# Optimization experiments

Hardware: AMD Instinct MI355X
Metric: run time of the kernel (lower is better)

Reference implementation:

```python
import jax, jax.numpy as jnp
import numpy as np

B, S, R = 8192, 256, 8192  # gas cells, species, reactions


def setup_inputs() -> dict:
    key = jax.random.key(0)
    ks = jax.random.split(key, 10)
    abundances = jax.random.uniform(ks[0], (B, S), jnp.float32, 1e-12, 1.0)
    temperature = jax.random.uniform(ks[1], (B,), jnp.float32, 10.0, 300.0)
    cr_rate = jax.random.uniform(ks[2], (B,), jnp.float32, 0.1, 10.0)
    fuv_rate = jax.random.uniform(ks[3], (B,), jnp.float32, 0.1, 10.0)
    time = jnp.zeros((B,), jnp.float32)  # unused by the RHS, kept for signature parity
    incidence = jax.random.normal(ks[4], (S, R), jnp.float32)  # stoichiometry matrix
    alpha = jax.random.uniform(ks[5], (R,), jnp.float32, 1e-12, 1e-9)
    beta = jax.random.normal(ks[6], (R,), jnp.float32) * 0.5
    gamma = jax.random.uniform(ks[7], (R,), jnp.float32, 0.0, 100.0)
    # species index or S (== out-of-bounds sentinel -> fill_value 1.0, i.e. <2 reactants)
    reactant_multipliers = jax.random.randint(ks[8], (R, 2), 0, S + 1, jnp.int32)
    rtype = jax.random.randint(ks[9], (R,), 0, 3, jnp.int32)  # 0: Arrhenius, 1: CR, 2: FUV
    return {
        'time': time, 'abundances': abundances, 'temperature': temperature,
        'cr_rate': cr_rate, 'fuv_rate': fuv_rate, 'incidence': incidence,
        'alpha': alpha, 'beta': beta, 'gamma': gamma,
        'reactant_multipliers': reactant_multipliers, 'rtype': rtype,
    }


def _get_rates(temperature, cr_rate, fuv_rate, alpha, beta, gamma, rtype):
    # JNetwork.get_rates: hstack of per-reaction rate terms -> (B, R)
    T = temperature[:, None]                                      # (B, 1)
    k_arr = alpha * jnp.exp(beta * jnp.log(T / 300.0) - gamma / T)  # Arrhenius
    k_cr = alpha * cr_rate[:, None]                               # cosmic-ray driven
    k_fuv = alpha * jnp.exp(-gamma) * fuv_rate[:, None]           # FUV photorate
    return jnp.where(rtype == 0, k_arr, jnp.where(rtype == 1, k_cr, k_fuv))


def reference(time, abundances, temperature, cr_rate, fuv_rate,
              incidence, alpha, beta, gamma, reactant_multipliers, rtype):
    rates = _get_rates(temperature, cr_rate, fuv_rate, alpha, beta, gamma, rtype)
    # multiply_rates_by_abundance: gather reactant abundances (mode='drop',
    # fill_value=1.0) and reduce with a product over the 2 reactant slots.
    ones_col = jnp.ones((abundances.shape[0], 1), abundances.dtype)
    ab_pad = jnp.concatenate([abundances, ones_col], axis=1)      # (B, S+1), col S == 1.0
    prod = ab_pad[:, reactant_multipliers[:, 0]] * ab_pad[:, reactant_multipliers[:, 1]]  # (B, R)
    flux = rates * prod                                           # (B, R)
    # incidence @ rates, batched: (S, R) x (B, R) -> (B, S)
    return jnp.einsum('sr,br->bs', incidence, flux)
```

## Files before the change

kernel.cpp:

```cpp
#include <hip/hip_runtime.h>
#include <stdint.h>

typedef __bf16 bf16;
typedef __bf16 bf16x8 __attribute__((ext_vector_type(8)));
typedef float  f32x4  __attribute__((ext_vector_type(4)));

#if __has_builtin(__builtin_amdgcn_exp2f)
#define EXP2F(x) __builtin_amdgcn_exp2f(x)
#else
#define EXP2F(x) exp2f(x)
#endif

constexpr int Bn = 8192, Sn = 256, Rn = 8192;
constexpr int BM = 64, BK = 32, KP = 4;
constexpr int KLEN = Rn / KP;
constexpr int NC = KLEN / BK;

__global__ __launch_bounds__(256) void prep_all(
    const float* __restrict__ inc, bf16* __restrict__ incb,
    const float* __restrict__ alpha, const float* __restrict__ beta,
    const float* __restrict__ gam, const int* __restrict__ rm, const int* __restrict__ rtype,
    float4* __restrict__ params, const float* __restrict__ temp,
    const float* __restrict__ cr, const float* __restrict__ fuv, float4* __restrict__ perb) {
  __shared__ __align__(16) float row_lds[8192];
  __shared__ unsigned short perm_lds[8192];
  __shared__ int c0[256], c1[256], c2[256];
  const int g = blockIdx.x, t = threadIdx.x;

  int* rt = (int*)row_lds;
  {
    const int4* src = (const int4*)rtype;
    int4* dst = (int4*)rt;
#pragma unroll
    for (int i = 0; i < 8; ++i) dst[i * 256 + t] = src[i * 256 + t];
  }
  __syncthreads();

  int ty[32];
  int l0 = 0, l1 = 0, l2 = 0;
#pragma unroll
  for (int i = 0; i < 32; ++i) {
    int v = rt[i * 256 + t];
    ty[i] = v;
    l0 += (v == 0); l1 += (v == 1); l2 += (v == 2);
  }
  c0[t] = l0; c1[t] = l1; c2[t] = l2;
  __syncthreads();
  for (int off = 1; off < 256; off <<= 1) {
    int a = (t >= off) ? c0[t - off] : 0;
    int b = (t >= off) ? c1[t - off] : 0;
    int c = (t >= off) ? c2[t - off] : 0;
    __syncthreads();
    c0[t] += a; c1[t] += b; c2[t] += c;
    __syncthreads();
  }
  const int tot0 = c0[255], tot1 = c1[255];
  int o0 = c0[t] - l0;
  int o1 = tot0 + c1[t] - l1;
  int o2 = tot0 + tot1 + c2[t] - l2;
#pragma unroll
  for (int i = 0; i < 32; ++i) {
    int v = ty[i];
    int pos = (v == 0) ? o0++ : ((v == 1) ? o1++ : o2++);
    perm_lds[pos] = (unsigned short)(i * 256 + t);
  }
  __syncthreads();

  if (g < 32) {
    int p = g * 256 + t;
    int r = perm_lds[p];
    float a = alpha[r], be = beta[r], gm = gam[r];
    int tv = rt[r];
    int i0 = rm[2 * r], i1 = rm[2 * r + 1];
    float x, P = 0.0f, Q = 0.0f;
    if (tv == 0) { x = __log2f(a); P = be; Q = gm; }
    else if (tv == 1) { x = a; }
    else { x = a * expf(-gm); }
    uint32_t bits = (uint32_t)i0 | ((uint32_t)i1 << 10) | ((uint32_t)tv << 20);
    params[p] = make_float4(x, P, Q, __uint_as_float(bits));
  } else if (g < 64) {
    int b = (g - 32) * 256 + t;
    float T = temp[b];
    perb[b] = make_float4(__log2f(T * (1.0f / 300.0f)), 1.4426950408889634f / T,
                          cr[b], fuv[b]);
  }
  __syncthreads();

  {
    const float4* src = (const float4*)(inc + ((size_t)g << 13));
    float4* dst = (float4*)row_lds;
#pragma unroll
    for (int i = 0; i < 8; ++i) dst[i * 256 + t] = src[i * 256 + t];
  }
  __syncthreads();

  const unsigned short* pp = perm_lds + t * 32;
  bf16* outp = incb + ((size_t)t * 256 + g) * 32;
#pragma unroll
  for (int k8 = 0; k8 < 4; ++k8) {
    bf16x8 o;
#pragma unroll
    for (int i = 0; i < 8; ++i) o[i] = (bf16)row_lds[pp[k8 * 8 + i]];
    *(bf16x8*)(outp + k8 * 8) = o;
  }
}

__global__ __launch_bounds__(256, 2) void flux_gemm(
    const float* __restrict__ abund, const float4* __restrict__ perb,
    const float4* __restrict__ params, const bf16* __restrict__ incb,
    float* __restrict__ partial) {
  __shared__ bf16 ab_lds[257 * 64];
  __shared__ bf16 flux_lds[2][64 * BK];

  const int tid  = threadIdx.x;
  const int lane = tid & 63;
  const int w    = tid >> 6;
  const int ws   = __builtin_amdgcn_readfirstlane(w);
  const int x   = blockIdx.x & 7;
  const int jb  = blockIdx.x >> 3;
  const int kp  = x & 3;
  const int m0g = (jb * 2 + (x >> 2)) * BM;
  const int kstart = kp * KLEN;
  const int r16 = lane & 15, q = lane >> 4;
  const int sw16 = (r16 >> 1) & 3;
  const int fsw  = w ^ ((lane >> 1) & 3);

  float4 pr0[8];
  {
    const float4* pw = params + kstart + ws * 8;
#pragma unroll
    for (int j = 0; j < 8; ++j) pr0[j] = pw[j];
  }

  {
    int bsub = tid >> 2;
    int scol = (tid & 3) * 64;
    const float* rowp = abund + (size_t)(m0g + bsub) * Sn + scol;
#pragma unroll
    for (int j = 0; j < 16; ++j) {
      float4 v = *(const float4*)(rowp + j * 4);
      int s = scol + j * 4;
      ab_lds[(s + 0) * 64 + bsub] = (bf16)v.x;
      ab_lds[(s + 1) * 64 + bsub] = (bf16)v.y;
      ab_lds[(s + 2) * 64 + bsub] = (bf16)v.z;
      ab_lds[(s + 3) * 64 + bsub] = (bf16)v.w;
    }
    if (tid < 64) ab_lds[256 * 64 + tid] = (bf16)1.0f;
  }

  float4 pb = perb[m0g + lane];
  const float l2t = pb.x, nitv = -pb.y, crv = pb.z, fuvv = pb.w;

  auto flux_tile = [&](int buf, const float4* pr) {
    uint32_t b0 = __builtin_amdgcn_readfirstlane(__float_as_uint(pr[0].w));
    uint32_t b7 = __builtin_amdgcn_readfirstlane(__float_as_uint(pr[7].w));
    uint32_t t0 = b0 >> 20, t7 = b7 >> 20;
    bf16x8 fv;
    if (t0 == 0 && t7 == 0) {
#pragma unroll
      for (int j = 0; j < 8; ++j) {
        uint32_t bits = __builtin_amdgcn_readfirstlane(__float_as_uint(pr[j].w));
        int i0 = (int)(bits & 1023), i1 = (int)((bits >> 10) & 1023);
        float a0 = (float)ab_lds[i0 * 64 + lane];
        float a1 = (float)ab_lds[i1 * 64 + lane];
        float v = EXP2F(fmaf(pr[j].y, l2t, fmaf(pr[j].z, nitv, pr[j].x)));
        fv[j] = (bf16)(v * (a0 * a1));
      }
    } else if (t0 == t7) {
      float mv = (t0 == 1) ? crv : fuvv;
#pragma unroll
      for (int j = 0; j < 8; ++j) {
        uint32_t bits = __builtin_amdgcn_readfirstlane(__float_as_uint(pr[j].w));
        int i0 = (int)(bits & 1023), i1 = (int)((bits >> 10) & 1023);
        float a0 = (float)ab_lds[i0 * 64 + lane];
        float a1 = (float)ab_lds[i1 * 64 + lane];
        fv[j] = (bf16)((pr[j].x * mv) * (a0 * a1));
      }
    } else {
#pragma unroll
      for (int j = 0; j < 8; ++j) {
        uint32_t bits = __builtin_amdgcn_readfirstlane(__float_as_uint(pr[j].w));
        int i0 = (int)(bits & 1023), i1 = (int)((bits >> 10) & 1023), ms = (int)(bits >> 20);
        float a0 = (float)ab_lds[i0 * 64 + lane];
        float a1 = (float)ab_lds[i1 * 64 + lane];
        float ve = EXP2F(fmaf(pr[j].y, l2t, fmaf(pr[j].z, nitv, pr[j].x)));
        float vm = pr[j].x * ((ms == 1) ? crv : fuvv);
        float v = (ms == 0) ? ve : vm;
        fv[j] = (bf16)(v * (a0 * a1));
      }
    }
    *(bf16x8*)(flux_lds[buf] + lane * BK + fsw * 8) = fv;
  };

  auto load_params = [&](int chunk, float4* pr) {
    const float4* pw = params + kstart + chunk * BK + ws * 8;
#pragma unroll
    for (int j = 0; j < 8; ++j) pr[j] = pw[j];
  };

  const bf16* bbase = incb + (size_t)(kstart / BK) * 8192 + (w * 64 + r16) * BK + q * 8;
  auto load_bfr = [&](int chunk, bf16x8* bfr) {
    const bf16* bp = bbase + (size_t)chunk * 8192;
#pragma unroll
    for (int nt = 0; nt < 4; ++nt)
      bfr[nt] = *(const bf16x8*)(bp + nt * (16 * BK));
  };

  auto do_mfma = [&](f32x4 (*acc)[4], const bf16x8* af, const bf16x8* bfr) {
    __builtin_amdgcn_s_setprio(1);
#pragma unroll
    for (int mt = 0; mt < 4; ++mt)
#pragma unroll
      for (int nt = 0; nt < 4; ++nt)
        acc[mt][nt] = __builtin_amdgcn_mfma_f32_16x16x32_bf16(af[mt], bfr[nt], acc[mt][nt], 0, 0, 0);
    __builtin_amdgcn_s_setprio(0);
  };

  __syncthreads();

  flux_tile(0, pr0);

  float4 prE[8], prO[8];
  bf16x8 bfrA[4], bfrB[4];
  load_bfr(0, bfrA);

  f32x4 acc[4][4];
#pragma unroll
  for (int i = 0; i < 4; ++i)
#pragma unroll
    for (int j = 0; j < 4; ++j) acc[i][j] = (f32x4)0.0f;

  for (int c = 0; c < NC; c += 2) {
    __syncthreads();
    load_params(c + 1, prE);
    bf16x8 afA[4];
#pragma unroll
    for (int mt = 0; mt < 4; ++mt)
      afA[mt] = *(const bf16x8*)(flux_lds[0] + (mt * 16 + r16) * BK + (q ^ sw16) * 8);
    load_bfr(c + 1, bfrB);
    flux_tile(1, prE);
    do_mfma(acc, afA, bfrA);

    __syncthreads();
    const int c2 = (c + 2 < NC) ? c + 2 : 0;
    load_params(c2, prO);
    bf16x8 afB[4];
#pragma unroll
    for (int mt = 0; mt < 4; ++mt)
      afB[mt] = *(const bf16x8*)(flux_lds[1] + (mt * 16 + r16) * BK + (q ^ sw16) * 8);
    load_bfr(c2, bfrA);
    if (c + 2 < NC) flux_tile(0, prO);
    do_mfma(acc, afB, bfrB);
  }

  float* pout = partial + (size_t)kp * Bn * Sn;
#pragma unroll
  for (int mt = 0; mt < 4; ++mt)
#pragma unroll
    for (int nt = 0; nt < 4; ++nt) {
      int col = w * 64 + nt * 16 + r16;
      int row = m0g + mt * 16 + q * 4;
#pragma unroll
      for (int rg = 0; rg < 4; ++rg)
        pout[(size_t)(row + rg) * Sn + col] = acc[mt][nt][rg];
    }
}

__global__ __launch_bounds__(256) void reduce_k(const float* __restrict__ partial,
                                               float* __restrict__ out) {
  size_t i = ((size_t)blockIdx.x * 256 + threadIdx.x) * 4;
  constexpr size_t NS = (size_t)Bn * Sn;
  float4 a = *(const float4*)(partial + i);
  float4 b = *(const float4*)(partial + NS + i);
  float4 c = *(const float4*)(partial + 2 * NS + i);
  float4 d = *(const float4*)(partial + 3 * NS + i);
  float4 r;
  r.x = (a.x + b.x) + (c.x + d.x);
  r.y = (a.y + b.y) + (c.y + d.y);
  r.z = (a.z + b.z) + (c.z + d.z);
  r.w = (a.w + b.w) + (c.w + d.w);
  *(float4*)(out + i) = r;
}

extern "C" void kernel_launch(void* const* d_in, const int* in_sizes, int n_in,
                              void* d_out, int out_size, void* d_ws, size_t ws_size,
                              hipStream_t stream) {
  const float* abund = (const float*)d_in[1];
  const float* temp  = (const float*)d_in[2];
  const float* cr    = (const float*)d_in[3];
  const float* fuv   = (const float*)d_in[4];
  const float* inc   = (const float*)d_in[5];
  const float* alpha = (const float*)d_in[6];
  const float* beta  = (const float*)d_in[7];
  const float* gam   = (const float*)d_in[8];
  const int*   rm    = (const int*)d_in[9];
  const int*   rty   = (const int*)d_in[10];
  float* out = (float*)d_out;

  float4* params  = (float4*)d_ws;
  float4* perb    = params + Rn;
  bf16*   incb    = (bf16*)(perb + Bn);
  float*  partial = (float*)(incb + (size_t)Sn * Rn);

  prep_all<<<256, 256, 0, stream>>>(inc, incb, alpha, beta, gam, rm, rty,
                                    params, temp, cr, fuv, perb);
  flux_gemm<<<(Bn / BM) * KP, 256, 0, stream>>>(abund, perb, params, incb, partial);
  reduce_k<<<(Bn * Sn) / 1024, 256, 0, stream>>>(partial, out);
}
```

Measured before the change: 154.2 us.

## Prefetch rate parameters one chunk further ahead and use lgkm-only barriers

Parameter loads now run two chunks ahead of their use instead of one, so the global-load latency of the per-reaction params is hidden behind a full MFMA and flux step. The loop barriers switch from __syncthreads to an explicit lgkmcnt(0) wait plus s_barrier. That barrier waits only on LDS and scalar traffic, so in-flight global loads of params and B fragments can cross it. Register pressure rises a little from keeping the extra param buffer live. Indices are clamped at the tail, which adds a few redundant loads.

```diff
diff --git a/kernel.cpp b/kernel.cpp
--- a/kernel.cpp
+++ b/kernel.cpp
@@ -10,6 +10,12 @@
 #else
 #define EXP2F(x) exp2f(x)
 #endif
+
+#define LGKM_BARRIER()                                    \
+  do {                                                    \
+    asm volatile("s_waitcnt lgkmcnt(0)" ::: "memory");    \
+    __builtin_amdgcn_s_barrier();                         \
+  } while (0)
 
 constexpr int Bn = 8192, Sn = 256, Rn = 8192;
 constexpr int BM = 64, BK = 32, KP = 4;
@@ -125,12 +131,14 @@
   const int sw16 = (r16 >> 1) & 3;
   const int fsw  = w ^ ((lane >> 1) & 3);
 
-  float4 pr0[8];
-  {
-    const float4* pw = params + kstart + ws * 8;
-#pragma unroll
-    for (int j = 0; j < 8; ++j) pr0[j] = pw[j];
-  }
+  auto load_params = [&](int chunk, float4* pr) {
+    const float4* pw = params + kstart + chunk * BK + ws * 8;
+#pragma unroll
+    for (int j = 0; j < 8; ++j) pr[j] = pw[j];
+  };
+
+  float4 prE[8], prO[8];
+  load_params(0, prE);
 
   {
     int bsub = tid >> 2;
@@ -192,12 +200,6 @@
     *(bf16x8*)(flux_lds[buf] + lane * BK + fsw * 8) = fv;
   };
 
-  auto load_params = [&](int chunk, float4* pr) {
-    const float4* pw = params + kstart + chunk * BK + ws * 8;
-#pragma unroll
-    for (int j = 0; j < 8; ++j) pr[j] = pw[j];
-  };
-
   const bf16* bbase = incb + (size_t)(kstart / BK) * 8192 + (w * 64 + r16) * BK + q * 8;
   auto load_bfr = [&](int chunk, bf16x8* bfr) {
     const bf16* bp = bbase + (size_t)chunk * 8192;
@@ -218,10 +220,10 @@
 
   __syncthreads();
 
-  flux_tile(0, pr0);
-
-  float4 prE[8], prO[8];
+  flux_tile(0, prE);
+
   bf16x8 bfrA[4], bfrB[4];
+  load_params(1, prO);
   load_bfr(0, bfrA);
 
   f32x4 acc[4][4];
@@ -231,25 +233,33 @@
     for (int j = 0; j < 4; ++j) acc[i][j] = (f32x4)0.0f;
 
   for (int c = 0; c < NC; c += 2) {
-    __syncthreads();
-    load_params(c + 1, prE);
+    LGKM_BARRIER();
     bf16x8 afA[4];
 #pragma unroll
     for (int mt = 0; mt < 4; ++mt)
       afA[mt] = *(const bf16x8*)(flux_lds[0] + (mt * 16 + r16) * BK + (q ^ sw16) * 8);
+    {
+      const int cp = (c + 2 < NC) ? c + 2 : NC - 1;
+      load_params(cp, prE);
+    }
     load_bfr(c + 1, bfrB);
-    flux_tile(1, prE);
+    flux_tile(1, prO);
     do_mfma(acc, afA, bfrA);
 
-    __syncthreads();
-    const int c2 = (c + 2 < NC) ? c + 2 : 0;
-    load_params(c2, prO);
+    LGKM_BARRIER();
     bf16x8 afB[4];
 #pragma unroll
     for (int mt = 0; mt < 4; ++mt)
       afB[mt] = *(const bf16x8*)(flux_lds[1] + (mt * 16 + r16) * BK + (q ^ sw16) * 8);
-    load_bfr(c2, bfrA);
-    if (c + 2 < NC) flux_tile(0, prO);
+    {
+      const int cp = (c + 3 < NC) ? c + 3 : NC - 1;
+      load_params(cp, prO);
+    }
+    {
+      const int cp = (c + 2 < NC) ? c + 2 : NC - 1;
+      load_bfr(cp, bfrA);
+    }
+    if (c + 2 < NC) flux_tile(0, prE);
     do_mfma(acc, afB, bfrB);
   }
 
```

After: 154.8 us. Within noise of the previous version (+0.4%).
